# Performance work log

Hardware: AMD Instinct MI355X
Metric: run time of the kernel (lower is better)

## Reference

```python
import jax, jax.numpy as jnp
import numpy as np

N_E = 1024
E_DIM = 256
BETA = 0.25
BATCH = 131072


def setup_inputs() -> dict:
    key = jax.random.key(0)
    k1, k2 = jax.random.split(key)
    z = jax.random.normal(k1, (BATCH, E_DIM), dtype=jnp.float32)
    # matches nn.Embedding init uniform_(-1/n_e, 1/n_e)
    emb_weight = jax.random.uniform(k2, (N_E, E_DIM), dtype=jnp.float32,
                                    minval=-1.0 / N_E, maxval=1.0 / N_E)
    return {"z": z, "emb_weight": emb_weight}


def reference(z, emb_weight):
    # z: [B, e_dim] (the module's unsqueeze/permute/view is an identity reshape)
    # squared L2 distances: [B, n_e]
    d = (jnp.sum(z * z, axis=1, keepdims=True)
         + jnp.sum(emb_weight * emb_weight, axis=1)
         - 2.0 * jnp.matmul(z, emb_weight.T))
    min_encoding_indices = jnp.argmin(d, axis=1)            # [B]
    min_encodings = jax.nn.one_hot(min_encoding_indices, N_E, dtype=z.dtype)  # [B, n_e]
    z_q = jnp.matmul(min_encodings, emb_weight)             # [B, e_dim]

    sg = jax.lax.stop_gradient
    loss = jnp.mean((sg(z_q) - z) ** 2) + BETA * jnp.mean((z_q - sg(z)) ** 2)

    # straight-through estimator
    z_q_ste = z + sg(z_q - z)

    e_mean = jnp.mean(min_encodings, axis=0)                # [n_e]
    perplexity = jnp.exp(-jnp.sum(e_mean * jnp.log(e_mean + 1e-10)))

    return (z_q_ste, loss, min_encoding_indices[:, None], perplexity)
```

## Files before the change

kernel.cpp:

```cpp
#include <hip/hip_runtime.h>

typedef __attribute__((ext_vector_type(8))) __bf16 bf16x8;
typedef __attribute__((ext_vector_type(4))) float f32x4;
typedef __attribute__((ext_vector_type(8))) unsigned short u16x8;

#define B_ROWS 131072
#define EDIM   256
#define N_E    1024
#define BMR    64
#define CHUNKS 32
#define CAP    16

#define OUT1 ((size_t)B_ROWS * EDIM)
#define OUT2 (OUT1 + 1)
#define OUT3 (OUT2 + B_ROWS)

#define WS_EMBT  0
#define WS_ESQ   524288
#define WS_COUNT 528384
#define WS_LOSS  532480

__device__ __forceinline__ unsigned short f2bf(float f) {
    unsigned u = __float_as_uint(f);
    return (unsigned short)((u + 0x7FFFu + ((u >> 16) & 1u)) >> 16);
}
__device__ __forceinline__ unsigned encf(float f) {
    unsigned u = __float_as_uint(f);
    return u ^ (unsigned)(((int)u >> 31) | 0x80000000);
}
__device__ __forceinline__ float decf(unsigned x) {
    return (x & 0x80000000u) ? __uint_as_float(x ^ 0x80000000u)
                             : __uint_as_float(~x);
}
__device__ __forceinline__ float med3f(float a, float b, float c) {
#if __has_builtin(__builtin_amdgcn_fmed3f)
    return __builtin_amdgcn_fmed3f(a, b, c);
#else
    return fmaxf(fminf(a, b), fminf(fmaxf(a, b), c));
#endif
}

__device__ inline float pw128_sq(const float* p) {
    float4 v0 = *(const float4*)p, v1 = *(const float4*)(p + 4);
    float r[8];
    r[0] = __fmul_rn(v0.x, v0.x); r[1] = __fmul_rn(v0.y, v0.y);
    r[2] = __fmul_rn(v0.z, v0.z); r[3] = __fmul_rn(v0.w, v0.w);
    r[4] = __fmul_rn(v1.x, v1.x); r[5] = __fmul_rn(v1.y, v1.y);
    r[6] = __fmul_rn(v1.z, v1.z); r[7] = __fmul_rn(v1.w, v1.w);
    for (int i = 8; i < 128; i += 8) {
        v0 = *(const float4*)(p + i); v1 = *(const float4*)(p + i + 4);
        r[0] = __fadd_rn(r[0], __fmul_rn(v0.x, v0.x));
        r[1] = __fadd_rn(r[1], __fmul_rn(v0.y, v0.y));
        r[2] = __fadd_rn(r[2], __fmul_rn(v0.z, v0.z));
        r[3] = __fadd_rn(r[3], __fmul_rn(v0.w, v0.w));
        r[4] = __fadd_rn(r[4], __fmul_rn(v1.x, v1.x));
        r[5] = __fadd_rn(r[5], __fmul_rn(v1.y, v1.y));
        r[6] = __fadd_rn(r[6], __fmul_rn(v1.z, v1.z));
        r[7] = __fadd_rn(r[7], __fmul_rn(v1.w, v1.w));
    }
    float s01 = __fadd_rn(r[0], r[1]), s23 = __fadd_rn(r[2], r[3]);
    float s45 = __fadd_rn(r[4], r[5]), s67 = __fadd_rn(r[6], r[7]);
    return __fadd_rn(__fadd_rn(s01, s23), __fadd_rn(s45, s67));
}

__device__ inline float exact_d(const float* zp, const float* ep, float zsq, float eq) {
    const float4* z4 = (const float4*)zp;
    const float4* e4 = (const float4*)ep;
    float acc = 0.f;
#pragma unroll 8
    for (int k = 0; k < 64; ++k) {
        float4 a = z4[k], b = e4[k];
        acc = __fmaf_rn(a.x, b.x, acc);
        acc = __fmaf_rn(a.y, b.y, acc);
        acc = __fmaf_rn(a.z, b.z, acc);
        acc = __fmaf_rn(a.w, b.w, acc);
    }
    return __fsub_rn(__fadd_rn(zsq, eq), 2.0f * acc);
}

__global__ void prep_emb(const float* __restrict__ emb,
                         unsigned short* __restrict__ embT,
                         float* __restrict__ esqg)
{
    int n = blockIdx.x, t = threadIdx.x;
    const float4 v = ((const float4*)(emb + (size_t)n * EDIM))[t];
    ushort4 o = { f2bf(v.x), f2bf(v.y), f2bf(v.z), f2bf(v.w) };
    int g = t >> 1, j0 = (t & 1) * 4;
    *(ushort4*)(embT + ((size_t)g * N_E + n) * 8 + j0) = o;
    if (t < 2) {
        float h = pw128_sq(emb + (size_t)n * EDIM + 128 * t);
        float ho = __shfl_xor(h, 1);
        if (t == 0) esqg[n] = __fadd_rn(h, ho);
    }
}

__global__ __launch_bounds__(256, 3) void vq_main(
    const float* __restrict__ z, const float* __restrict__ emb,
    const unsigned short* __restrict__ embT, const float* __restrict__ esqg,
    float* __restrict__ out, unsigned int* __restrict__ count,
    double* __restrict__ lossSum)
{
    __shared__ float esq_s[N_E];
    __shared__ float zsq_s[BMR], S_s[BMR], thr_s[BMR];
    __shared__ unsigned long long wd64[2][BMR];
    __shared__ unsigned cnt[BMR];
    __shared__ unsigned short list[BMR][CAP];
    __shared__ int rowbest[BMR];
    __shared__ double red4[4];
    __shared__ unsigned long long fb4[4];

    const int tid  = threadIdx.x;
    const int blk  = blockIdx.x;
    const int lane = tid & 63;
    const int w    = tid >> 6;
    const int col  = lane & 15;
    const int quad = lane >> 4;
    const int nt   = w >> 1;
    const int mh   = w & 1;

    const float* zb = z + (size_t)blk * BMR * EDIM;

    for (int i = tid; i < N_E; i += 256) esq_s[i] = esqg[i];
    if (tid < BMR) cnt[tid] = 0u;

    bf16x8 afr[2][8];
#pragma unroll
    for (int mti = 0; mti < 2; ++mti) {
        int row = 32 * mh + 16 * mti + col;
#pragma unroll
        for (int ks = 0; ks < 8; ++ks) {
            const float* p = zb + row * EDIM + ((ks * 4 + quad) << 3);
            float4 a0 = *(const float4*)p;
            float4 a1 = *(const float4*)(p + 4);
            u16x8 t = { f2bf(a0.x), f2bf(a0.y), f2bf(a0.z), f2bf(a0.w),
                        f2bf(a1.x), f2bf(a1.y), f2bf(a1.z), f2bf(a1.w) };
            afr[mti][ks] = *(bf16x8*)&t;
        }
    }

    if (tid < 128) {
        int row = tid >> 1, half = tid & 1;
        const float* p = zb + row * EDIM + half * 128;
        float h = pw128_sq(p);
        const float4* p4 = (const float4*)p;
        float4 sv = {0.f, 0.f, 0.f, 0.f};
#pragma unroll
        for (int jj = 0; jj < 32; ++jj) {
            float4 vv = p4[jj];
            sv.x += fabsf(vv.x); sv.y += fabsf(vv.y);
            sv.z += fabsf(vv.z); sv.w += fabsf(vv.w);
        }
        float sa = (sv.x + sv.y) + (sv.z + sv.w);
        float ho = __shfl_xor(h, 1);
        float so = __shfl_xor(sa, 1);
        if (half == 0) {
            zsq_s[row] = __fadd_rn(h, ho);
            S_s[row]   = (sa + so) * 1.001f;
        }
    }
    __syncthreads();

    int koff[8];
#pragma unroll
    for (int ks = 0; ks < 8; ++ks)
        koff[ks] = (((ks * 4 + quad) << 10) + nt * 16 + col) * 8;

    float bd1[2][4], bd2[2][4], bd3[2][4];
    int   cp_[2][4];
#pragma unroll
    for (int mti = 0; mti < 2; ++mti)
#pragma unroll
        for (int r = 0; r < 4; ++r) {
            bd1[mti][r] = INFINITY; bd2[mti][r] = INFINITY; bd3[mti][r] = INFINITY;
            cp_[mti][r] = 0;
        }

#pragma unroll 2
    for (int c = 0; c < CHUNKS; ++c) {
        const unsigned short* cb = embT + (c << 8);
        u16x8 bfr[8];
#pragma unroll
        for (int ks = 0; ks < 8; ++ks)
            bfr[ks] = *(const u16x8*)(cb + koff[ks]);
        f32x4 acc0 = {0.f, 0.f, 0.f, 0.f}, acc1 = {0.f, 0.f, 0.f, 0.f};
#pragma unroll
        for (int ks = 0; ks < 8; ++ks) {
            bf16x8 b = *(bf16x8*)&bfr[ks];
            acc0 = __builtin_amdgcn_mfma_f32_16x16x32_bf16(afr[0][ks], b, acc0, 0, 0, 0);
            acc1 = __builtin_amdgcn_mfma_f32_16x16x32_bf16(afr[1][ks], b, acc1, 0, 0, 0);
        }
        const int codeN = (c << 5) + nt * 16 + col;
        const float eqv = esq_s[codeN];
#pragma unroll
        for (int mti = 0; mti < 2; ++mti)
#pragma unroll
            for (int r = 0; r < 4; ++r) {
                float s = __fmaf_rn(-2.0f, (mti ? acc1[r] : acc0[r]), eqv);
                bool lt1 = s < bd1[mti][r];
                bool lt2 = s < bd2[mti][r];
                bd3[mti][r] = med3f(s, bd2[mti][r], bd3[mti][r]);
                bd2[mti][r] = med3f(s, bd1[mti][r], bd2[mti][r]);
                bd1[mti][r] = fminf(s, bd1[mti][r]);
                int cpo = cp_[mti][r];
                int low = cpo & 0xFFFF;
                cp_[mti][r] = lt1 ? (codeN | (low << 16))
                                  : (lt2 ? (low | (codeN << 16)) : cpo);
            }
    }

#pragma unroll
    for (int mti = 0; mti < 2; ++mti)
#pragma unroll
        for (int r = 0; r < 4; ++r) {
            unsigned long long kk =
                ((unsigned long long)encf(bd1[mti][r]) << 32)
                | (unsigned)(cp_[mti][r] & 0xFFFF);
#pragma unroll
            for (int msk = 1; msk <= 8; msk <<= 1) {
                unsigned long long o = __shfl_xor(kk, msk);
                if (o < kk) kk = o;
            }
            if (col == 0) wd64[nt][32 * mh + 16 * mti + 4 * quad + r] = kk;
        }
    __syncthreads();
    if (tid < BMR) {
        unsigned long long a = wd64[0][tid], b = wd64[1][tid];
        unsigned long long mn = a < b ? a : b;
        thr_s[tid] = decf((unsigned)(mn >> 32)) + (S_s[tid] * (1.0f / 131072.0f) + 1e-4f);
    }
    __syncthreads();

#pragma unroll
    for (int mti = 0; mti < 2; ++mti)
#pragma unroll
        for (int r = 0; r < 4; ++r) {
            int row = 32 * mh + 16 * mti + 4 * quad + r;
            float th = thr_s[row];
            if (__builtin_expect(bd1[mti][r] <= th, 0)) {
                unsigned i = atomicAdd(&cnt[row], 1u);
                if (i < CAP) list[row][i] = (unsigned short)(cp_[mti][r] & 0xFFFF);
            }
            if (__builtin_expect(bd2[mti][r] <= th, 0)) {
                unsigned i = atomicAdd(&cnt[row], 1u);
                if (i < CAP) list[row][i] = (unsigned short)((unsigned)cp_[mti][r] >> 16);
            }
            if (__builtin_expect(bd3[mti][r] <= th, 0))
                atomicAdd(&cnt[row], 1000u);
        }
    __syncthreads();

    {
        int row = tid >> 2, j = tid & 3;
        int cn = (int)cnt[row];
        unsigned long long bkey = ~0ull;
        float zq = zsq_s[row];
        const float* zrow = zb + row * EDIM;
        if (cn <= CAP) {
            for (int i = j; i < cn; i += 4) {
                int n = (int)list[row][i];
                float d = exact_d(zrow, emb + (size_t)n * EDIM, zq, esq_s[n]);
                unsigned long long k2 = ((unsigned long long)encf(d) << 32) | (unsigned)n;
                if (k2 < bkey) bkey = k2;
            }
        }
#pragma unroll
        for (int m = 1; m <= 2; m <<= 1) {
            unsigned long long o = __shfl_xor(bkey, m);
            if (o < bkey) bkey = o;
        }
        if (j == 0) rowbest[row] = (cn <= CAP) ? (int)(bkey & 0xFFFFFFFFu) : -1;
    }
    __syncthreads();

    for (int r = 0; r < BMR; ++r) {
        if (rowbest[r] != -1) continue;
        const float* zr = zb + r * EDIM;
        float zqr = zsq_s[r];
        unsigned long long k = ~0ull;
        for (int ci = 0; ci < 4; ++ci) {
            int n = tid + ci * 256;
            float d = exact_d(zr, emb + (size_t)n * EDIM, zqr, esq_s[n]);
            unsigned long long k2 = ((unsigned long long)encf(d) << 32) | (unsigned)n;
            if (k2 < k) k = k2;
        }
#pragma unroll
        for (int msk = 1; msk <= 32; msk <<= 1) {
            unsigned long long o = __shfl_xor(k, msk);
            if (o < k) k = o;
        }
        if (lane == 0) fb4[w] = k;
        __syncthreads();
        if (tid == 0) {
            unsigned long long m0 = fb4[0] < fb4[1] ? fb4[0] : fb4[1];
            unsigned long long m1 = fb4[2] < fb4[3] ? fb4[2] : fb4[3];
            rowbest[r] = (int)((m0 < m1 ? m0 : m1) & 0xFFFFFFFFu);
        }
        __syncthreads();
    }

    {
        const int row = tid >> 2, q = tid & 3;
        const size_t grow = (size_t)blk * BMR + row;
        const int bn = rowbest[row];
        const float4* zp4 = (const float4*)(zb + row * EDIM);
        const float4* ebr = (const float4*)(emb + (size_t)bn * EDIM);
        float4* outr = (float4*)(out + grow * EDIM);
        double lacc = 0.0;
#pragma unroll
        for (int i = 0; i < 16; ++i) {
            int k4 = q + i * 4;
            float4 zv = zp4[k4];
            float4 ev = ebr[k4];
            float4 o; float sd;
            sd = __fsub_rn(ev.x, zv.x); o.x = __fadd_rn(zv.x, sd); lacc += (double)__fmul_rn(sd, sd);
            sd = __fsub_rn(ev.y, zv.y); o.y = __fadd_rn(zv.y, sd); lacc += (double)__fmul_rn(sd, sd);
            sd = __fsub_rn(ev.z, zv.z); o.z = __fadd_rn(zv.z, sd); lacc += (double)__fmul_rn(sd, sd);
            sd = __fsub_rn(ev.w, zv.w); o.w = __fadd_rn(zv.w, sd); lacc += (double)__fmul_rn(sd, sd);
            outr[k4] = o;
        }
        if (q == 0) {
            out[OUT2 + grow] = (float)bn;
            atomicAdd(&count[bn], 1u);
        }
#pragma unroll
        for (int msk = 1; msk <= 32; msk <<= 1) lacc += __shfl_xor(lacc, msk);
        if (lane == 0) red4[w] = lacc;
        __syncthreads();
        if (tid == 0) atomicAdd(lossSum, red4[0] + red4[1] + red4[2] + red4[3]);
    }
}

__global__ void vq_finalize(const unsigned int* __restrict__ count,
                            const double* __restrict__ lossSum,
                            float* __restrict__ out)
{
    __shared__ double red[1024];
    int t = threadIdx.x;
    double em = (double)count[t] * (1.0 / 131072.0);
    red[t] = em * log(em + 1e-10);
    __syncthreads();
    for (int s = 512; s > 0; s >>= 1) {
        if (t < s) red[t] += red[t + s];
        __syncthreads();
    }
    if (t == 0) {
        out[OUT3] = (float)exp(-red[0]);
        double m = lossSum[0] * (1.0 / 33554432.0);
        out[OUT1] = (float)(1.25 * m);
    }
}

extern "C" void kernel_launch(void* const* d_in, const int* in_sizes, int n_in,
                              void* d_out, int out_size, void* d_ws, size_t ws_size,
                              hipStream_t stream) {
    const float* z   = (const float*)d_in[0];
    const float* emb = (const float*)d_in[1];
    float* out = (float*)d_out;

    unsigned short* embT = (unsigned short*)((char*)d_ws + WS_EMBT);
    float* esqg          = (float*)((char*)d_ws + WS_ESQ);
    unsigned int* count  = (unsigned int*)((char*)d_ws + WS_COUNT);
    double* lossSum      = (double*)((char*)d_ws + WS_LOSS);

    hipMemsetAsync((char*)d_ws + WS_COUNT, 0, 4104, stream);
    prep_emb<<<N_E, 64, 0, stream>>>(emb, embT, esqg);
    vq_main<<<B_ROWS / BMR, 256, 0, stream>>>(z, emb, embT, esqg, out, count, lossSum);
    vq_finalize<<<1, 1024, 0, stream>>>(count, lossSum, out);
}
```

Measured before the change: 341.9 us.

## Split output and loss epilogue out of search kernel into separate kernel

Moves the z_q_ste write and loss accumulation from the search kernel into a new vq_output kernel. That kernel reads the best index back from the output buffer, uses 32 rows per block and 8 threads per row. It also changes the search kernel's launch bounds from 3 to 2 waves per EU. The goal is to shorten the search kernel's register and tail cost and let the memory-bound epilogue run at full occupancy. In exchange, z is read from HBM a second time and there is one more kernel launch.

```diff
diff --git a/kernel.cpp b/kernel.cpp
--- a/kernel.cpp
+++ b/kernel.cpp
@@ -10,6 +10,7 @@
 #define BMR    64
 #define CHUNKS 32
 #define CAP    16
+#define OROWS  32
 
 #define OUT1 ((size_t)B_ROWS * EDIM)
 #define OUT2 (OUT1 + 1)
@@ -94,11 +95,10 @@
     }
 }
 
-__global__ __launch_bounds__(256, 3) void vq_main(
+__global__ __launch_bounds__(256, 2) void vq_search(
     const float* __restrict__ z, const float* __restrict__ emb,
     const unsigned short* __restrict__ embT, const float* __restrict__ esqg,
-    float* __restrict__ out, unsigned int* __restrict__ count,
-    double* __restrict__ lossSum)
+    float* __restrict__ out, unsigned int* __restrict__ count)
 {
     __shared__ float esq_s[N_E];
     __shared__ float zsq_s[BMR], S_s[BMR], thr_s[BMR];
@@ -106,7 +106,6 @@
     __shared__ unsigned cnt[BMR];
     __shared__ unsigned short list[BMR][CAP];
     __shared__ int rowbest[BMR];
-    __shared__ double red4[4];
     __shared__ unsigned long long fb4[4];
 
     const int tid  = threadIdx.x;
@@ -298,36 +297,46 @@
         __syncthreads();
     }
 
-    {
-        const int row = tid >> 2, q = tid & 3;
-        const size_t grow = (size_t)blk * BMR + row;
-        const int bn = rowbest[row];
-        const float4* zp4 = (const float4*)(zb + row * EDIM);
-        const float4* ebr = (const float4*)(emb + (size_t)bn * EDIM);
-        float4* outr = (float4*)(out + grow * EDIM);
-        double lacc = 0.0;
-#pragma unroll
-        for (int i = 0; i < 16; ++i) {
-            int k4 = q + i * 4;
-            float4 zv = zp4[k4];
-            float4 ev = ebr[k4];
-            float4 o; float sd;
-            sd = __fsub_rn(ev.x, zv.x); o.x = __fadd_rn(zv.x, sd); lacc += (double)__fmul_rn(sd, sd);
-            sd = __fsub_rn(ev.y, zv.y); o.y = __fadd_rn(zv.y, sd); lacc += (double)__fmul_rn(sd, sd);
-            sd = __fsub_rn(ev.z, zv.z); o.z = __fadd_rn(zv.z, sd); lacc += (double)__fmul_rn(sd, sd);
-            sd = __fsub_rn(ev.w, zv.w); o.w = __fadd_rn(zv.w, sd); lacc += (double)__fmul_rn(sd, sd);
-            outr[k4] = o;
-        }
-        if (q == 0) {
-            out[OUT2 + grow] = (float)bn;
-            atomicAdd(&count[bn], 1u);
-        }
-#pragma unroll
-        for (int msk = 1; msk <= 32; msk <<= 1) lacc += __shfl_xor(lacc, msk);
-        if (lane == 0) red4[w] = lacc;
-        __syncthreads();
-        if (tid == 0) atomicAdd(lossSum, red4[0] + red4[1] + red4[2] + red4[3]);
-    }
+    if (tid < BMR) {
+        int bn = rowbest[tid];
+        out[OUT2 + (size_t)blk * BMR + tid] = (float)bn;
+        atomicAdd(&count[bn], 1u);
+    }
+}
+
+__global__ void vq_output(const float* __restrict__ z, const float* __restrict__ emb,
+                          float* __restrict__ out, double* __restrict__ lossSum)
+{
+    __shared__ double red4s[4];
+    const int tid = threadIdx.x;
+    const int blk = blockIdx.x;
+    const int lane = tid & 63;
+    const int w   = tid >> 6;
+    const int row = tid >> 3;
+    const int q   = tid & 7;
+    const size_t grow = (size_t)blk * OROWS + row;
+    const int bn = (int)out[OUT2 + grow];
+    const float4* zp4 = (const float4*)(z + grow * EDIM);
+    const float4* ebr = (const float4*)(emb + (size_t)bn * EDIM);
+    float4* outr = (float4*)(out + grow * EDIM);
+    double lacc = 0.0;
+#pragma unroll
+    for (int i = 0; i < 8; ++i) {
+        int k4 = q + i * 8;
+        float4 zv = zp4[k4];
+        float4 ev = ebr[k4];
+        float4 o; float sd;
+        sd = __fsub_rn(ev.x, zv.x); o.x = __fadd_rn(zv.x, sd); lacc += (double)__fmul_rn(sd, sd);
+        sd = __fsub_rn(ev.y, zv.y); o.y = __fadd_rn(zv.y, sd); lacc += (double)__fmul_rn(sd, sd);
+        sd = __fsub_rn(ev.z, zv.z); o.z = __fadd_rn(zv.z, sd); lacc += (double)__fmul_rn(sd, sd);
+        sd = __fsub_rn(ev.w, zv.w); o.w = __fadd_rn(zv.w, sd); lacc += (double)__fmul_rn(sd, sd);
+        outr[k4] = o;
+    }
+#pragma unroll
+    for (int msk = 1; msk <= 32; msk <<= 1) lacc += __shfl_xor(lacc, msk);
+    if (lane == 0) red4s[w] = lacc;
+    __syncthreads();
+    if (tid == 0) atomicAdd(lossSum, red4s[0] + red4s[1] + red4s[2] + red4s[3]);
 }
 
 __global__ void vq_finalize(const unsigned int* __restrict__ count,
@@ -364,6 +373,7 @@
 
     hipMemsetAsync((char*)d_ws + WS_COUNT, 0, 4104, stream);
     prep_emb<<<N_E, 64, 0, stream>>>(emb, embT, esqg);
-    vq_main<<<B_ROWS / BMR, 256, 0, stream>>>(z, emb, embT, esqg, out, count, lossSum);
+    vq_search<<<B_ROWS / BMR, 256, 0, stream>>>(z, emb, embT, esqg, out, count);
+    vq_output<<<B_ROWS / OROWS, 256, 0, stream>>>(z, emb, out, lossSum);
     vq_finalize<<<1, 1024, 0, stream>>>(count, lossSum, out);
 }
```

Result: slower. 386.2 us (+12.9%).
